# Kernel tuning notes

Hardware: AMD Instinct MI355X
Metric: run time of the kernel (lower is better)

## Reference

```python
import jax, jax.numpy as jnp
import numpy as np

B, F, H, OUT, S = 32768, 256, 128, 64, 6
RELAX, EPS, BN_EPS = 1.5, 1e-05, 1e-05
SQRT_HALF = 0.7071067811865476


def _bn(h, g, b):
    # training-mode BatchNorm1d: biased batch statistics over dim 0
    m = h.mean(axis=0)
    v = h.var(axis=0)
    return (h - m) * jax.lax.rsqrt(v + BN_EPS) * g + b


def _tfrm(x, W, g, b, glu_act=True):
    h = _bn(x @ W, g, b)
    if glu_act:
        d = h.shape[1] // 2
        h = h[:, :d] * jax.nn.sigmoid(h[:, d:])
    return h


def setup_inputs() -> dict:
    key = jax.random.key(0)
    ks = jax.random.split(key, 6)
    f32 = jnp.float32
    return {
        "x": jax.random.normal(ks[0], (B, F), f32),
        "enc_g": jnp.ones((F,), f32), "enc_b": jnp.zeros((F,), f32),
        "W1": jax.random.normal(ks[1], (F, 2 * H), f32) * 0.05,
        "g1": jnp.ones((2 * H,), f32), "b1": jnp.zeros((2 * H,), f32),
        "W2": jax.random.normal(ks[2], (H, 2 * H), f32) * 0.05,
        "g2": jnp.ones((2 * H,), f32), "b2": jnp.zeros((2 * H,), f32),
        "W3": jax.random.normal(ks[3], (S, H, 2 * H), f32) * 0.05,
        "g3": jnp.ones((S, 2 * H), f32), "b3": jnp.zeros((S, 2 * H), f32),
        "W4": jax.random.normal(ks[4], (S, H, 2 * H), f32) * 0.05,
        "g4": jnp.ones((S, 2 * H), f32), "b4": jnp.zeros((S, 2 * H), f32),
        "Wc": jax.random.normal(ks[5], (S - 1, OUT, F), f32) * 0.05,
        "gc": jnp.ones((S - 1, F), f32), "bc": jnp.zeros((S - 1, F), f32),
    }


def reference(x, enc_g, enc_b, W1, g1, b1, W2, g2, b2, W3, g3, b3,
              W4, g4, b4, Wc, gc, bc):
    x = _bn(x, enc_g, enc_b)                      # [B, F]
    masked = x
    compl = jnp.ones((x.shape[0], F), x.dtype)    # complementary aggregated mask
    agg_out, agg_entropy = [], []
    for ni in range(S):
        h = _tfrm(masked, W1, g1, b1)                             # [B, H]
        h = (_tfrm(h, W2, g2, b2) + h) * SQRT_HALF
        h = (_tfrm(h, W3[ni], g3[ni], b3[ni]) + h) * SQRT_HALF
        h = (_tfrm(h, W4[ni], g4[ni], b4[ni]) + h) * SQRT_HALF
        if ni > 0:
            # NOTE: source uses x (not h) here -- replicated faithfully
            agg_out.append(jax.nn.relu(x[:, :OUT]))
        fc = h[:, OUT:]                                           # [B, OUT]
        if ni < S - 1:
            coef = _tfrm(fc, Wc[ni], gc[ni], bc[ni], glu_act=False)  # [B, F]
            mask_values = jax.nn.softmax(coef * compl, axis=1)
            compl = compl * (RELAX - mask_values)
            agg_entropy.append(
                jnp.mean(jnp.sum(-mask_values * jnp.log(mask_values + EPS), axis=1))
                / (S - 1))
            masked = mask_values * x
    out = jnp.sum(jnp.stack(agg_out, axis=0), axis=0)   # [B, OUT]
    entropy = jnp.sum(jnp.stack(agg_entropy))           # scalar
    return (out, entropy)
```

## Files before the change

### kernel.cpp

```cpp
#include <hip/hip_runtime.h>
#include <math.h>

#define BSZ   32768
#define FDIM  256
#define HDIM  128
#define OUTD  64
#define SQRT_HALF 0.70710678118654752f
#define BN_EPS 1e-5f
#define SM_EPS 1e-5f
#define INV_B (1.0f / 32768.0f)
#define NCPY  8
#define SLOT  (NCPY * 512)
#define GRID  1024

#define SWZ(r, cb) ((((r) << 9) + (cb)) ^ (((r) & 7) << 4))

typedef __attribute__((ext_vector_type(8))) short bf16x8;
typedef __attribute__((ext_vector_type(4))) short bf16x4;
typedef __attribute__((ext_vector_type(4))) float f32x4;

__device__ __forceinline__ float b2f(unsigned short u) {
    return __uint_as_float(((unsigned int)u) << 16);
}
__device__ __forceinline__ unsigned short f2b(float f) {
    unsigned int u = __float_as_uint(f);
    u += 0x7fff + ((u >> 16) & 1);
    return (unsigned short)(u >> 16);
}

__device__ __forceinline__ void async16(const void* g, void* l) {
    __builtin_amdgcn_global_load_lds(
        (const __attribute__((address_space(1))) void*)(uintptr_t)g,
        (__attribute__((address_space(3))) void*)(unsigned int)(uintptr_t)l,
        16, 0, 0);
}

__device__ __forceinline__ float cload(const float* p) {
    return __hip_atomic_load(p, __ATOMIC_RELAXED, __HIP_MEMORY_SCOPE_AGENT);
}
__device__ __forceinline__ void catomic_add(float* p, float v) {
    float old = __hip_atomic_fetch_add(p, v, __ATOMIC_RELAXED, __HIP_MEMORY_SCOPE_AGENT);
    asm volatile("" :: "v"(old));
}

__device__ inline float waveMaxAll(float v) {
#pragma unroll
    for (int m = 32; m > 0; m >>= 1) v = fmaxf(v, __shfl_xor(v, m, 64));
    return v;
}
__device__ inline float waveSumAll(float v) {
#pragma unroll
    for (int m = 32; m > 0; m >>= 1) v += __shfl_xor(v, m, 64);
    return v;
}

__device__ __forceinline__ void grid_sync_nf(unsigned int* arr, unsigned int* rel,
                                             unsigned int gen, int bid, int tid) {
    __syncthreads();
    if (tid == 0)
        __hip_atomic_fetch_add(&arr[(bid & 63) << 5], 1u,
                               __ATOMIC_RELAXED, __HIP_MEMORY_SCOPE_AGENT);
    if (bid == 0) {
        if (tid < 64) {
            unsigned int* p = &arr[tid << 5];
            long spin = 0;
            while (__hip_atomic_load(p, __ATOMIC_RELAXED, __HIP_MEMORY_SCOPE_AGENT) < gen * 16u) {
                if (++spin > (1L << 24)) break;
                __builtin_amdgcn_s_sleep(1);
            }
        }
        asm volatile("" ::: "memory");
        __syncthreads();
        if (tid == 0)
            __hip_atomic_store(rel, gen, __ATOMIC_RELAXED, __HIP_MEMORY_SCOPE_AGENT);
    } else {
        if (tid == 0) {
            long spin = 0;
            while (__hip_atomic_load(rel, __ATOMIC_RELAXED, __HIP_MEMORY_SCOPE_AGENT) < gen) {
                if (++spin > (1L << 24)) break;
                __builtin_amdgcn_s_sleep(2);
            }
        }
        asm volatile("" ::: "memory");
    }
    __syncthreads();
}

__device__ __forceinline__ void stage_B(short* Bs, const unsigned short* __restrict__ Wt,
                                        int K, int k0, int wave, int lane) {
    const int sr = lane >> 2;
    const int sc = (lane & 3) * 8;
#pragma unroll
    for (int t = 0; t < 4; ++t) {
        const int wr = wave * 64 + t * 16 + sr;
        async16(Wt + (size_t)wr * K + k0 + sc, (void*)(Bs + (wave * 4 + t) * 512 + lane * 8));
    }
}

__device__ __forceinline__ void gemm_core(const short* buf, short* Bs,
                                          const unsigned short* __restrict__ Wt, int K,
                                          int wave, int lane, f32x4 (&acc)[2][4]) {
    const int fm = lane & 15;
    const int fq = (lane >> 4) * 8;
#pragma unroll
    for (int i = 0; i < 2; ++i)
#pragma unroll
        for (int j = 0; j < 4; ++j)
            acc[i][j] = (f32x4){0.f, 0.f, 0.f, 0.f};

    __syncthreads();

    for (int k0 = 0; k0 < K; k0 += 32) {
        asm volatile("s_waitcnt vmcnt(0)" ::: "memory");
        bf16x8 af[2], bfr[4];
#pragma unroll
        for (int i = 0; i < 2; ++i)
            af[i] = *(const bf16x8*)((const char*)buf + SWZ(i * 16 + fm, (k0 + fq) * 2));
#pragma unroll
        for (int j = 0; j < 4; ++j)
            bfr[j] = *(const bf16x8*)(Bs + (wave * 64 + j * 16 + fm) * 32 + fq);
#pragma unroll
        for (int i = 0; i < 2; ++i)
#pragma unroll
            for (int j = 0; j < 4; ++j)
                acc[i][j] = __builtin_amdgcn_mfma_f32_16x16x32_bf16(af[i], bfr[j], acc[i][j], 0, 0, 0);
        if (k0 + 32 < K) {
            asm volatile("s_waitcnt lgkmcnt(0)" ::: "memory");
            __builtin_amdgcn_sched_barrier(0);
            stage_B(Bs, Wt, K, k0 + 32, wave, lane);
        }
    }
    __syncthreads();
}

__device__ __forceinline__ void stage_epilogue(f32x4 (&acc)[2][4], short* buf,
                                               float* redS, float* redQ,
                                               float* __restrict__ statsOut,
                                               int wave, int lane, int tid, int bcp) {
    const int fm = lane & 15;
    const int row4 = (lane >> 4) * 4;
    const int ocol = wave * 64 + fm;
#pragma unroll
    for (int i = 0; i < 2; ++i)
#pragma unroll
        for (int j = 0; j < 4; ++j)
#pragma unroll
            for (int r = 0; r < 4; ++r)
                *(short*)((char*)buf + SWZ(row4 + i * 16 + r, (ocol + j * 16) * 2)) =
                    (short)f2b(acc[i][j][r]);

#pragma unroll
    for (int j = 0; j < 4; ++j) {
        float s = 0.f, q = 0.f;
#pragma unroll
        for (int i = 0; i < 2; ++i)
#pragma unroll
            for (int r = 0; r < 4; ++r) {
                float v = acc[i][j][r];
                s += v; q += v * v;
            }
        s += __shfl_xor(s, 16, 64); s += __shfl_xor(s, 32, 64);
        q += __shfl_xor(q, 16, 64); q += __shfl_xor(q, 32, 64);
        if (lane < 16) {
            redS[wave * 64 + j * 16 + lane] = s;
            redQ[wave * 64 + j * 16 + lane] = q;
        }
    }
    __syncthreads();
    catomic_add(&statsOut[bcp + tid], redS[tid]);
    catomic_add(&statsOut[bcp + 256 + tid], redQ[tid]);
}

__device__ __forceinline__ void build_tbl_glu(const float* __restrict__ st,
                                              const float* __restrict__ pg,
                                              const float* __restrict__ pb,
                                              int colOff, int K, int tid, float* tbl) {
    if (tid < K) {
        const int ch = colOff + tid;
        const int cg = ch + 128;
        float sA = 0.f, qA = 0.f, sG = 0.f, qG = 0.f;
#pragma unroll
        for (int cp = 0; cp < NCPY; ++cp) {
            const float* p = st + cp * 512;
            sA += cload(p + ch); qA += cload(p + 256 + ch);
            sG += cload(p + cg); qG += cload(p + 256 + cg);
        }
        float ma = sA * INV_B, va = qA * INV_B - ma * ma;
        float scA = pg[ch] * rsqrtf(va + BN_EPS);
        tbl[tid] = scA; tbl[K + tid] = pb[ch] - ma * scA;
        float mg = sG * INV_B, vg = qG * INV_B - mg * mg;
        float scG = pg[cg] * rsqrtf(vg + BN_EPS);
        tbl[2 * K + tid] = scG; tbl[3 * K + tid] = pb[cg] - mg * scG;
    }
    __syncthreads();
}

__device__ __forceinline__ void build_tbl_mask(const float* __restrict__ st,
                                               const float* __restrict__ gcp,
                                               const float* __restrict__ bcp_,
                                               int tid, float* tbl) {
    float s = 0.f, q = 0.f;
#pragma unroll
    for (int cp = 0; cp < NCPY; ++cp) {
        s += cload(st + cp * 512 + tid);
        q += cload(st + cp * 512 + 256 + tid);
    }
    float mean = s * INV_B, var = q * INV_B - mean * mean;
    float scl = gcp[tid] * rsqrtf(var + BN_EPS);
    tbl[tid] = scl;
    tbl[256 + tid] = bcp_[tid] - mean * scl;
    __syncthreads();
}

template <int K, bool RES, bool WH, int RB>
__device__ __forceinline__ void glu_prologue(short* buf, const float* tbl,
                                             int tid, int colOff, bf16x4* h) {
    const int ar = tid >> 3;
    const int ac = (tid & 7) * 4;
#pragma unroll
    for (int c = 0; c < K / 32; ++c) {
        const int kk = c * 32 + ac;
        bf16x4 lo = *(const bf16x4*)((const char*)buf + SWZ(ar, (colOff + kk) * 2));
        bf16x4 hi = *(const bf16x4*)((const char*)buf + SWZ(ar, (colOff + kk + 128) * 2));
        float4 a0 = *(const float4*)&tbl[kk];
        float4 h0 = *(const float4*)&tbl[K + kk];
        float4 g0 = *(const float4*)&tbl[2 * K + kk];
        float4 s0 = *(const float4*)&tbl[3 * K + kk];
        const float scA[4] = {a0.x, a0.y, a0.z, a0.w};
        const float shA[4] = {h0.x, h0.y, h0.z, h0.w};
        const float scG[4] = {g0.x, g0.y, g0.z, g0.w};
        const float shG[4] = {s0.x, s0.y, s0.z, s0.w};
        bf16x4 o4;
#pragma unroll
        for (int e = 0; e < 4; ++e) {
            float na = b2f((unsigned short)lo[e]) * scA[e] + shA[e];
            float ng = b2f((unsigned short)hi[e]) * scG[e] + shG[e];
            float v = na * (1.0f / (1.0f + __expf(-ng)));
            if (RES) v = (v + b2f((unsigned short)h[RB + c][e])) * SQRT_HALF;
            o4[e] = (short)f2b(v);
        }
        *(bf16x4*)((char*)buf + SWZ(ar, kk * 2)) = o4;
        if (WH) h[c] = o4;
    }
}

template <int MODE>
__device__ __forceinline__ void mask_phase(short* buf, const float* tbl,
                                           const unsigned short* __restrict__ xb,
                                           unsigned short* cmpl, float* ent, float* went,
                                           int tid, int wave, int lane, int row0, int bid) {
    const int r = tid >> 3;
    const int cq = tid & 7;
    const size_t grow = (size_t)(row0 + r) * 256;

    float l[32];
    float mx = -1e30f;
#pragma unroll
    for (int e = 0; e < 4; ++e) {
        const int c = cq * 32 + e * 8;
        bf16x8 pv = *(const bf16x8*)((const char*)buf + SWZ(r, c * 2));
        bf16x8 cv;
        if (MODE != 0) cv = *(const bf16x8*)(cmpl + grow + c);
        float4 s0 = *(const float4*)&tbl[c], s1 = *(const float4*)&tbl[c + 4];
        float4 h0 = *(const float4*)&tbl[256 + c], h1 = *(const float4*)&tbl[256 + c + 4];
        const float* sp0 = (const float*)&s0; const float* sp1 = (const float*)&s1;
        const float* hp0 = (const float*)&h0; const float* hp1 = (const float*)&h1;
#pragma unroll
        for (int t = 0; t < 8; ++t) {
            float scl = (t < 4) ? sp0[t] : sp1[t - 4];
            float shf = (t < 4) ? hp0[t] : hp1[t - 4];
            float cl = (MODE != 0) ? b2f((unsigned short)cv[t]) : 1.0f;
            float v = (b2f((unsigned short)pv[t]) * scl + shf) * cl;
            l[e * 8 + t] = v;
            mx = fmaxf(mx, v);
        }
    }
    mx = fmaxf(mx, __shfl_xor(mx, 1, 64));
    mx = fmaxf(mx, __shfl_xor(mx, 2, 64));
    mx = fmaxf(mx, __shfl_xor(mx, 4, 64));

    float ssum = 0.f;
#pragma unroll
    for (int i = 0; i < 32; ++i) { l[i] = __expf(l[i] - mx); ssum += l[i]; }
    ssum += __shfl_xor(ssum, 1, 64);
    ssum += __shfl_xor(ssum, 2, 64);
    ssum += __shfl_xor(ssum, 4, 64);
    const float inv = 1.0f / ssum;

    float et = 0.f;
#pragma unroll
    for (int e = 0; e < 4; ++e) {
        const int c = cq * 32 + e * 8;
        bf16x8 xv, cv2;
        if (MODE != 2) xv = *(const bf16x8*)(xb + grow + c);
        if (MODE == 1) cv2 = *(const bf16x8*)(cmpl + grow + c);
        bf16x8 mo, co;
#pragma unroll
        for (int t = 0; t < 8; ++t) {
            float m = l[e * 8 + t] * inv;
            et -= m * __logf(m + SM_EPS);
            if (MODE != 2) {
                float cl = (MODE == 1) ? b2f((unsigned short)cv2[t]) : 1.0f;
                co[t] = (short)f2b(cl * (1.5f - m));
                mo[t] = (short)f2b(m * b2f((unsigned short)xv[t]));
            }
        }
        if (MODE != 2) {
            *(bf16x8*)(cmpl + grow + c) = co;
            *(bf16x8*)((char*)buf + SWZ(r, c * 2)) = mo;
        }
    }
    et += __shfl_xor(et, 1, 64);
    et += __shfl_xor(et, 2, 64);
    et += __shfl_xor(et, 4, 64);
    float wet = waveSumAll(et) * 0.125f;
    if (lane == 0) went[wave] = wet;
    __syncthreads();
    if (tid == 0) {
        float v = went[0] + went[1] + went[2] + went[3];
        catomic_add(&ent[(bid & 255) << 5], v * (INV_B * 0.2f));
    }
}

__global__ __launch_bounds__(256, 4) void mega(
    const float* __restrict__ x,
    const float* __restrict__ enc_g, const float* __restrict__ enc_b,
    const float* __restrict__ g1, const float* __restrict__ b1,
    const float* __restrict__ g2, const float* __restrict__ b2,
    const float* __restrict__ g3, const float* __restrict__ b3,
    const float* __restrict__ g4, const float* __restrict__ b4,
    const float* __restrict__ gc, const float* __restrict__ bc,
    const float* __restrict__ W1f, const float* __restrict__ W2f,
    const float* __restrict__ W3f, const float* __restrict__ W4f,
    const float* __restrict__ Wcf,
    unsigned short* __restrict__ W1t, unsigned short* __restrict__ W2t,
    unsigned short* __restrict__ W3t, unsigned short* __restrict__ W4t,
    unsigned short* __restrict__ Wct,
    unsigned short* __restrict__ xb, unsigned short* __restrict__ cmpl,
    float* __restrict__ stats, float* __restrict__ ent,
    unsigned int* __restrict__ bar,
    float* __restrict__ out)
{
    __shared__ short buf[32 * 256];
    __shared__ short Bs[256 * 32];
    __shared__ float redS[256], redQ[256];
    __shared__ float tbl[512];
    __shared__ float went[4];

    const int tid  = threadIdx.x;
    const int wave = tid >> 6;
    const int lane = tid & 63;
    const int bid  = blockIdx.x;
    const int row0 = bid * 32;
    const int bcp  = (bid & (NCPY - 1)) * 512;

    unsigned int* rel = bar + 64 * 32;
    unsigned int bgen = 0;
#define GSYNC() do { ++bgen; grid_sync_nf(bar, rel, bgen, bid, tid); } while (0)

    if (bid < 136) {
        const int m = bid >> 3, kz = bid & 7, n = tid;
        const float* src; unsigned short* dst; int K;
        if (m == 0)      { src = W1f;                        dst = W1t;               K = 256; }
        else if (m == 1) { src = W2f;                        dst = W2t;               K = 128; }
        else if (m < 7)  { int i = m - 2;  src = W3f + (size_t)i * 128 * 256; dst = W3t + (size_t)i * 32768; K = 128; }
        else if (m < 12) { int i = m - 7;  src = W4f + (size_t)i * 128 * 256; dst = W4t + (size_t)i * 32768; K = 128; }
        else             { int i = m - 12; src = Wcf + (size_t)i * 64 * 256;  dst = Wct + (size_t)i * 16384; K = 64; }
        const int k0 = kz * 32;
        if (k0 < K)
            for (int k = k0; k < k0 + 32; ++k)
                dst[(size_t)n * K + k] = f2b(src[(size_t)k * 256 + n]);
        __threadfence();
    }
    {
        float* red = (float*)buf;
        const int sub = wave;
        const int c4  = lane << 2;
        float s[4] = {0.f, 0.f, 0.f, 0.f}, q[4] = {0.f, 0.f, 0.f, 0.f};
#pragma unroll 8
        for (int i = 0; i < 8; ++i) {
            const int row = row0 + i * 4 + sub;
            float4 v = *(const float4*)(x + (size_t)row * 256 + c4);
            s[0] += v.x; q[0] += v.x * v.x;
            s[1] += v.y; q[1] += v.y * v.y;
            s[2] += v.z; q[2] += v.z * v.z;
            s[3] += v.w; q[3] += v.w * v.w;
        }
#pragma unroll
        for (int e = 0; e < 4; ++e) {
            red[sub * 512 + c4 + e] = s[e];
            red[sub * 512 + 256 + c4 + e] = q[e];
        }
        __syncthreads();
        float sS = red[tid] + red[512 + tid] + red[1024 + tid] + red[1536 + tid];
        float sQ = red[256 + tid] + red[768 + tid] + red[1280 + tid] + red[1792 + tid];
        catomic_add(&stats[bcp + tid], sS);
        catomic_add(&stats[bcp + 256 + tid], sQ);
    }
    GSYNC();

    stage_B(Bs, W1t, 256, 0, wave, lane);
    {
        float s = 0.f, q = 0.f;
#pragma unroll
        for (int cp = 0; cp < NCPY; ++cp) {
            s += cload(stats + cp * 512 + tid);
            q += cload(stats + cp * 512 + 256 + tid);
        }
        float mean = s * INV_B, var = q * INV_B - mean * mean;
        float scl = enc_g[tid] * rsqrtf(var + BN_EPS);
        tbl[tid] = scl;
        tbl[256 + tid] = enc_b[tid] - mean * scl;
    }
    __syncthreads();
    {
        const int r = tid >> 3, cq = tid & 7;
        const size_t grow = (size_t)(row0 + r) * 256;
#pragma unroll
        for (int e = 0; e < 4; ++e) {
            const int c = cq * 32 + e * 8;
            float4 xa = *(const float4*)(x + grow + c);
            float4 xc = *(const float4*)(x + grow + c + 4);
            const float xv[8] = {xa.x, xa.y, xa.z, xa.w, xc.x, xc.y, xc.z, xc.w};
            float4 s0 = *(const float4*)&tbl[c], s1 = *(const float4*)&tbl[c + 4];
            float4 f0 = *(const float4*)&tbl[256 + c], f1 = *(const float4*)&tbl[256 + c + 4];
            const float sc[8] = {s0.x, s0.y, s0.z, s0.w, s1.x, s1.y, s1.z, s1.w};
            const float sh[8] = {f0.x, f0.y, f0.z, f0.w, f1.x, f1.y, f1.z, f1.w};
            float n[8];
            bf16x8 o8;
#pragma unroll
            for (int t = 0; t < 8; ++t) {
                n[t] = xv[t] * sc[t] + sh[t];
                o8[t] = (short)f2b(n[t]);
            }
            *(bf16x8*)((char*)buf + SWZ(r, c * 2)) = o8;
            *(bf16x8*)(xb + grow + c) = o8;
            if (c < OUTD) {
                float4 o1 = make_float4(5.f * fmaxf(n[0], 0.f), 5.f * fmaxf(n[1], 0.f),
                                        5.f * fmaxf(n[2], 0.f), 5.f * fmaxf(n[3], 0.f));
                float4 o2 = make_float4(5.f * fmaxf(n[4], 0.f), 5.f * fmaxf(n[5], 0.f),
                                        5.f * fmaxf(n[6], 0.f), 5.f * fmaxf(n[7], 0.f));
                *(float4*)(out + (size_t)(row0 + r) * OUTD + c) = o1;
                *(float4*)(out + (size_t)(row0 + r) * OUTD + c + 4) = o2;
            }
        }
    }

    f32x4 acc[2][4];
    bf16x4 h[4];

    for (int ni = 0; ni < 5; ++ni) {
        float* s1 = stats + (size_t)(1 + ni * 5 + 0) * SLOT;
        float* s2 = stats + (size_t)(1 + ni * 5 + 1) * SLOT;
        float* s3 = stats + (size_t)(1 + ni * 5 + 2) * SLOT;
        float* s4 = stats + (size_t)(1 + ni * 5 + 3) * SLOT;
        float* s5 = stats + (size_t)(1 + ni * 5 + 4) * SLOT;

        if (ni > 0) {
            float* s5p = stats + (size_t)(1 + (ni - 1) * 5 + 4) * SLOT;
            build_tbl_mask(s5p, gc + (ni - 1) * 256, bc + (ni - 1) * 256, tid, tbl);
            if (ni == 1)
                mask_phase<0>(buf, tbl, xb, cmpl, ent, went, tid, wave, lane, row0, bid);
            else
                mask_phase<1>(buf, tbl, xb, cmpl, ent, went, tid, wave, lane, row0, bid);
        }
        gemm_core(buf, Bs, W1t, 256, wave, lane, acc);
        stage_epilogue(acc, buf, redS, redQ, s1, wave, lane, tid, bcp);
        stage_B(Bs, W2t, 128, 0, wave, lane);
        GSYNC();

        build_tbl_glu(s1, g1, b1, 0, 128, tid, tbl);
        glu_prologue<128, false, true, 0>(buf, tbl, tid, 0, h);
        gemm_core(buf, Bs, W2t, 128, wave, lane, acc);
        stage_epilogue(acc, buf, redS, redQ, s2, wave, lane, tid, bcp);
        stage_B(Bs, W3t + (size_t)ni * 32768, 128, 0, wave, lane);
        GSYNC();

        build_tbl_glu(s2, g2, b2, 0, 128, tid, tbl);
        glu_prologue<128, true, true, 0>(buf, tbl, tid, 0, h);
        gemm_core(buf, Bs, W3t + (size_t)ni * 32768, 128, wave, lane, acc);
        stage_epilogue(acc, buf, redS, redQ, s3, wave, lane, tid, bcp);
        stage_B(Bs, W4t + (size_t)ni * 32768, 128, 0, wave, lane);
        GSYNC();

        build_tbl_glu(s3, g3 + ni * 256, b3 + ni * 256, 0, 128, tid, tbl);
        glu_prologue<128, true, true, 0>(buf, tbl, tid, 0, h);
        gemm_core(buf, Bs, W4t + (size_t)ni * 32768, 128, wave, lane, acc);
        stage_epilogue(acc, buf, redS, redQ, s4, wave, lane, tid, bcp);
        stage_B(Bs, Wct + (size_t)ni * 16384, 64, 0, wave, lane);
        GSYNC();

        build_tbl_glu(s4, g4 + ni * 256, b4 + ni * 256, 64, 64, tid, tbl);
        glu_prologue<64, true, false, 2>(buf, tbl, tid, 64, h);
        gemm_core(buf, Bs, Wct + (size_t)ni * 16384, 64, wave, lane, acc);
        stage_epilogue(acc, buf, redS, redQ, s5, wave, lane, tid, bcp);
        if (ni < 4) stage_B(Bs, W1t, 256, 0, wave, lane);
        GSYNC();
    }

    build_tbl_mask(stats + (size_t)(1 + 4 * 5 + 4) * SLOT,
                   gc + 4 * 256, bc + 4 * 256, tid, tbl);
    mask_phase<2>(buf, tbl, xb, cmpl, ent, went, tid, wave, lane, row0, bid);
    GSYNC();

    if (bid == 0 && wave == 0) {
        float v = 0.f;
#pragma unroll
        for (int i = 0; i < 4; ++i) v += cload(ent + ((lane + 64 * i) << 5));
        v = waveSumAll(v);
        if (lane == 0) out[(size_t)BSZ * OUTD] = v;
    }
#undef GSYNC
}

__global__ __launch_bounds__(256) void prep_w(
    const float* __restrict__ W1, const float* __restrict__ W2,
    const float* __restrict__ W3, const float* __restrict__ W4,
    const float* __restrict__ Wc,
    unsigned short* __restrict__ W1t, unsigned short* __restrict__ W2t,
    unsigned short* __restrict__ W3t, unsigned short* __restrict__ W4t,
    unsigned short* __restrict__ Wct)
{
    const int m = blockIdx.x, kz = blockIdx.y, n = threadIdx.x;
    const float* src; unsigned short* dst; int K;
    if (m == 0)      { src = W1;                        dst = W1t;               K = 256; }
    else if (m == 1) { src = W2;                        dst = W2t;               K = 128; }
    else if (m < 7)  { int i = m - 2;  src = W3 + (size_t)i * 128 * 256; dst = W3t + (size_t)i * 32768; K = 128; }
    else if (m < 12) { int i = m - 7;  src = W4 + (size_t)i * 128 * 256; dst = W4t + (size_t)i * 32768; K = 128; }
    else             { int i = m - 12; src = Wc + (size_t)i * 64 * 256;  dst = Wct + (size_t)i * 16384; K = 64; }
    const int k0 = kz * 32;
    if (k0 >= K) return;
    for (int k = k0; k < k0 + 32; ++k)
        dst[(size_t)n * K + k] = f2b(src[(size_t)k * 256 + n]);
}

__global__ __launch_bounds__(256) void colstats(const float* __restrict__ X,
                                                float* __restrict__ st0) {
    __shared__ float red[4][512];
    const int sub = threadIdx.x >> 6;
    const int c4  = (threadIdx.x & 63) << 2;
    float s[4] = {0.f, 0.f, 0.f, 0.f}, q[4] = {0.f, 0.f, 0.f, 0.f};
#pragma unroll 8
    for (int i = 0; i < 8; ++i) {
        const int row = blockIdx.x * 32 + i * 4 + sub;
        float4 v = *(const float4*)(X + (size_t)row * 256 + c4);
        s[0] += v.x; q[0] += v.x * v.x;
        s[1] += v.y; q[1] += v.y * v.y;
        s[2] += v.z; q[2] += v.z * v.z;
        s[3] += v.w; q[3] += v.w * v.w;
    }
#pragma unroll
    for (int e = 0; e < 4; ++e) {
        red[sub][c4 + e] = s[e];
        red[sub][256 + c4 + e] = q[e];
    }
    __syncthreads();
    const int t = threadIdx.x;
    const int cp = (blockIdx.x & (NCPY - 1)) * 512;
    float sS = red[0][t] + red[1][t] + red[2][t] + red[3][t];
    float sQ = red[0][256 + t] + red[1][256 + t] + red[2][256 + t] + red[3][256 + t];
    atomicAdd(&st0[cp + t], sS);
    atomicAdd(&st0[cp + 256 + t], sQ);
}

__global__ __launch_bounds__(256) void norm_x(const float* __restrict__ x,
                                              const float* __restrict__ st0,
                                              const float* __restrict__ g,
                                              const float* __restrict__ b,
                                              unsigned short* __restrict__ xb,
                                              float* __restrict__ out) {
    const int i4 = blockIdx.x * 256 + threadIdx.x;
    const int row = i4 >> 6, c4 = (i4 & 63) << 2;
    float4 xv = *(const float4*)(x + (size_t)row * 256 + c4);
    float sS[4] = {0.f, 0.f, 0.f, 0.f}, sQ[4] = {0.f, 0.f, 0.f, 0.f};
#pragma unroll
    for (int cp = 0; cp < NCPY; ++cp) {
        float4 a = *(const float4*)&st0[cp * 512 + c4];
        float4 q = *(const float4*)&st0[cp * 512 + 256 + c4];
        sS[0] += a.x; sS[1] += a.y; sS[2] += a.z; sS[3] += a.w;
        sQ[0] += q.x; sQ[1] += q.y; sQ[2] += q.z; sQ[3] += q.w;
    }
    float4 gv = *(const float4*)&g[c4];
    float4 bv = *(const float4*)&b[c4];
    const float* xp = (const float*)&xv;
    const float* gp = (const float*)&gv; const float* bp = (const float*)&bv;
    float n[4];
    ushort4 ob;
    unsigned short* obp = (unsigned short*)&ob;
#pragma unroll
    for (int e = 0; e < 4; ++e) {
        float mean = sS[e] * INV_B;
        float var  = sQ[e] * INV_B - mean * mean;
        float sc   = gp[e] * rsqrtf(var + BN_EPS);
        float sh   = bp[e] - mean * sc;
        n[e] = xp[e] * sc + sh;
        obp[e] = f2b(n[e]);
    }
    *(ushort4*)(xb + (size_t)row * 256 + c4) = ob;
    if (c4 < OUTD) {
        float4 ov = make_float4(5.0f * fmaxf(n[0], 0.f), 5.0f * fmaxf(n[1], 0.f),
                                5.0f * fmaxf(n[2], 0.f), 5.0f * fmaxf(n[3], 0.f));
        *(float4*)(out + (size_t)row * OUTD + c4) = ov;
    }
}

__device__ __forceinline__ void gemm_epilogue(
    f32x4 (&acc)[2][4], int row0, int wave, int lane, int tid, int bcp,
    float* redS, float* redQ,
    unsigned short* __restrict__ Pout, float* __restrict__ statsOut)
{
    const int fm = lane & 15;
    const int orow = row0 + (lane >> 4) * 4;
    const int ocol = wave * 64 + fm;
#pragma unroll
    for (int i = 0; i < 2; ++i)
#pragma unroll
        for (int j = 0; j < 4; ++j)
#pragma unroll
            for (int r = 0; r < 4; ++r)
                Pout[(size_t)(orow + i * 16 + r) * 256 + (ocol + j * 16)] = f2b(acc[i][j][r]);

#pragma unroll
    for (int j = 0; j < 4; ++j) {
        float s = 0.f, q = 0.f;
#pragma unroll
        for (int i = 0; i < 2; ++i)
#pragma unroll
            for (int r = 0; r < 4; ++r) {
                float v = acc[i][j][r];
                s += v; q += v * v;
            }
        s += __shfl_xor(s, 16, 64); s += __shfl_xor(s, 32, 64);
        q += __shfl_xor(q, 16, 64); q += __shfl_xor(q, 32, 64);
        if (lane < 16) {
            redS[wave * 64 + j * 16 + lane] = s;
            redQ[wave * 64 + j * 16 + lane] = q;
        }
    }
    __syncthreads();
    atomicAdd(&statsOut[bcp + tid], redS[tid]);
    atomicAdd(&statsOut[bcp + 256 + tid], redQ[tid]);
}

__global__ __launch_bounds__(256) void gemm_bf16(
    const unsigned short* __restrict__ A,
    const unsigned short* __restrict__ Wt, int K,
    unsigned short* __restrict__ P,
    float* __restrict__ statsOut)
{
    __shared__ short As[32 * 32];
    __shared__ short Bs[256 * 32];
    __shared__ float redS[256], redQ[256];

    const int tid  = threadIdx.x;
    const int wave = tid >> 6;
    const int lane = tid & 63;
    const int row0 = blockIdx.x * 32;
    const int bcp  = (blockIdx.x & (NCPY - 1)) * 512;

    const int sr = lane >> 2;
    const int sc = (lane & 3) * 8;
    const int fm = lane & 15;
    const int fq = (lane >> 4) * 8;

    f32x4 acc[2][4];
// ... 271 lines not shown
            float4 h0 = *(const float4*)&tShA[kk];
            float4 g0 = *(const float4*)&tScG[kk];
            float4 s0 = *(const float4*)&tShG[kk];
            float scA[4] = {a0.x, a0.y, a0.z, a0.w};
            float shA[4] = {h0.x, h0.y, h0.z, h0.w};
            float scG[4] = {g0.x, g0.y, g0.z, g0.w};
            float shG[4] = {s0.x, s0.y, s0.z, s0.w};

            bf16x4 o4;
#pragma unroll
            for (int e = 0; e < 4; ++e) {
                float na = b2f((unsigned short)lo[e]) * scA[e] + shA[e];
                float ng = b2f((unsigned short)hi[e]) * scG[e] + shG[e];
                float v = na * (1.0f / (1.0f + __expf(-ng)));
                if (RES) v = (v + b2f((unsigned short)rv[e])) * SQRT_HALF;
                o4[e] = (short)f2b(v);
            }
            *(bf16x4*)(As + ar * 32 + ac) = o4;
            if (WRITE_H)
                *(bf16x4*)(hOut + grow * 128 + kk) = o4;
        }
        __syncthreads();

        bf16x8 af[2], bfr[4];
#pragma unroll
        for (int i = 0; i < 2; ++i)
            af[i] = *(const bf16x8*)(As + (i * 16 + fm) * 32 + fq);
#pragma unroll
        for (int j = 0; j < 4; ++j)
            bfr[j] = *(const bf16x8*)(Bs + (wave * 64 + j * 16 + fm) * 32 + fq);
#pragma unroll
        for (int i = 0; i < 2; ++i)
#pragma unroll
            for (int j = 0; j < 4; ++j)
                acc[i][j] = __builtin_amdgcn_mfma_f32_16x16x32_bf16(af[i], bfr[j], acc[i][j], 0, 0, 0);
        __syncthreads();
    }

    gemm_epilogue(acc, row0, wave, lane, tid, bcp, redS, redQ, Pout, statsOut);
}

__global__ __launch_bounds__(256) void coef_ent(const unsigned short* __restrict__ Pc,
                                                const float* __restrict__ stats,
                                                const float* __restrict__ gc,
                                                const float* __restrict__ bc,
                                                const unsigned short* __restrict__ cmpl,
                                                float* __restrict__ ent) {
    const int w    = threadIdx.x >> 6;
    const int lane = threadIdx.x & 63;
    const int row  = blockIdx.x * 4 + w;
    const int c    = lane << 2;
    __shared__ float went[4];

    float sS[4] = {0.f, 0.f, 0.f, 0.f}, sQ[4] = {0.f, 0.f, 0.f, 0.f};
#pragma unroll
    for (int cp = 0; cp < NCPY; ++cp) {
        float4 a = *(const float4*)&stats[cp * 512 + c];
        float4 q = *(const float4*)&stats[cp * 512 + 256 + c];
        sS[0] += a.x; sS[1] += a.y; sS[2] += a.z; sS[3] += a.w;
        sQ[0] += q.x; sQ[1] += q.y; sQ[2] += q.z; sQ[3] += q.w;
    }
    float4 gv = *(const float4*)&gc[c];
    float4 bv = *(const float4*)&bc[c];
    const float* gvv = (const float*)&gv; const float* bvv = (const float*)&bv;

    float scl[4], shf[4];
#pragma unroll
    for (int e = 0; e < 4; ++e) {
        float mean = sS[e] * INV_B, var = sQ[e] * INV_B - mean * mean;
        scl[e] = gvv[e] * rsqrtf(var + BN_EPS);
        shf[e] = bvv[e] - mean * scl[e];
    }

    const size_t idx = (size_t)row * 256 + c;
    ushort4 pu = *(const ushort4*)(Pc + idx);
    const unsigned short* puv = (const unsigned short*)&pu;
    ushort4 cu = *(const ushort4*)(cmpl + idx);
    const unsigned short* cuv = (const unsigned short*)&cu;

    float l[4];
#pragma unroll
    for (int e = 0; e < 4; ++e)
        l[e] = (b2f(puv[e]) * scl[e] + shf[e]) * b2f(cuv[e]);

    float mx = waveMaxAll(fmaxf(fmaxf(l[0], l[1]), fmaxf(l[2], l[3])));
    float e0 = __expf(l[0] - mx), e1 = __expf(l[1] - mx),
          e2 = __expf(l[2] - mx), e3 = __expf(l[3] - mx);
    float inv = 1.0f / waveSumAll(e0 + e1 + e2 + e3);

    float m[4] = {e0 * inv, e1 * inv, e2 * inv, e3 * inv};

    float et = -m[0] * __logf(m[0] + SM_EPS) - m[1] * __logf(m[1] + SM_EPS)
             - m[2] * __logf(m[2] + SM_EPS) - m[3] * __logf(m[3] + SM_EPS);
    et = waveSumAll(et);
    if (lane == 0) went[w] = et;
    __syncthreads();
    if (threadIdx.x == 0) {
        float v = went[0] + went[1] + went[2] + went[3];
        atomicAdd(&ent[(blockIdx.x & 255) << 5], v * (INV_B * 0.2f));
    }
}

__global__ __launch_bounds__(64) void write_ent(const float* __restrict__ ent,
                                                float* __restrict__ dst) {
    const int lane = threadIdx.x;
    float v = 0.f;
#pragma unroll
    for (int i = 0; i < 4; ++i) v += ent[(lane + 64 * i) << 5];
    v = waveSumAll(v);
    if (lane == 0) dst[0] = v;
}

extern "C" void kernel_launch(void* const* d_in, const int* in_sizes, int n_in,
                              void* d_out, int out_size, void* d_ws, size_t ws_size,
                              hipStream_t stream) {
    const float* x     = (const float*)d_in[0];
    const float* enc_g = (const float*)d_in[1];
    const float* enc_b = (const float*)d_in[2];
    const float* W1 = (const float*)d_in[3];
    const float* g1 = (const float*)d_in[4];
    const float* b1 = (const float*)d_in[5];
    const float* W2 = (const float*)d_in[6];
    const float* g2 = (const float*)d_in[7];
    const float* b2 = (const float*)d_in[8];
    const float* W3 = (const float*)d_in[9];
    const float* g3 = (const float*)d_in[10];
    const float* b3 = (const float*)d_in[11];
    const float* W4 = (const float*)d_in[12];
    const float* g4 = (const float*)d_in[13];
    const float* b4 = (const float*)d_in[14];
    const float* Wc = (const float*)d_in[15];
    const float* gc = (const float*)d_in[16];
    const float* bc = (const float*)d_in[17];
    float* out = (float*)d_out;

    const size_t NBF = (size_t)BSZ * FDIM;
    const size_t NBH = (size_t)BSZ * HDIM;

    unsigned short* xb     = (unsigned short*)d_ws;
    unsigned short* masked = xb + NBF;
    unsigned short* Pb1    = masked + NBF;
    unsigned short* h1     = Pb1 + NBF;
    unsigned short* h2     = h1 + NBH;
    unsigned short* h3     = h2 + NBH;
    unsigned short* cmpl   = h3 + NBH;
    unsigned short* W1t    = cmpl + NBF;
    unsigned short* W2t    = W1t + 65536;
    unsigned short* W3t    = W2t + 32768;
    unsigned short* W4t    = W3t + 163840;
    unsigned short* Wct    = W4t + 163840;
    float* stats = (float*)(Wct + 81920);
    float* ent   = stats + 26 * SLOT;
    unsigned int* bar = (unsigned int*)masked;

    unsigned short* Pb2 = masked;

    static int s_ok = -1;
    if (s_ok < 0) {
        int occ = 0, mpc = 0, dev = 0;
        hipGetDevice(&dev);
        hipDeviceProp_t prop;
        if (hipGetDeviceProperties(&prop, dev) == hipSuccess) mpc = prop.multiProcessorCount;
        if (hipOccupancyMaxActiveBlocksPerMultiprocessor(
                &occ, reinterpret_cast<const void*>(mega), 256, 0) != hipSuccess) occ = 0;
        s_ok = (occ >= 4 && occ * mpc >= GRID) ? 1 : 0;
    }

    hipMemsetAsync(stats, 0, (26 * SLOT + 256 * 32) * sizeof(float), stream);

    if (s_ok) {
        hipMemsetAsync(bar, 0, 65 * 32 * sizeof(unsigned int), stream);
        mega<<<GRID, 256, 0, stream>>>(
            x, enc_g, enc_b, g1, b1, g2, b2, g3, b3, g4, b4, gc, bc,
            W1, W2, W3, W4, Wc, W1t, W2t, W3t, W4t, Wct,
            xb, cmpl, stats, ent, bar, out);
        return;
    }

    prep_w<<<dim3(17, 8), 256, 0, stream>>>(W1, W2, W3, W4, Wc, W1t, W2t, W3t, W4t, Wct);
    colstats<<<1024, 256, 0, stream>>>(x, stats);
    norm_x<<<8192, 256, 0, stream>>>(x, stats, enc_g, enc_b, xb, out);

    for (int ni = 0; ni < 5; ++ni) {
        float* s1 = stats + (size_t)(1 + ni * 5 + 0) * SLOT;
        float* s2 = stats + (size_t)(1 + ni * 5 + 1) * SLOT;
        float* s3 = stats + (size_t)(1 + ni * 5 + 2) * SLOT;
        float* s4 = stats + (size_t)(1 + ni * 5 + 3) * SLOT;
        float* s5 = stats + (size_t)(1 + ni * 5 + 4) * SLOT;

        if (ni == 0) {
            gemm_bf16<<<1024, 256, 0, stream>>>(xb, W1t, 256, Pb1, s1);
        } else {
            float* s5p = stats + (size_t)(1 + (ni - 1) * 5 + 4) * SLOT;
            if (ni == 1)
                gemm_mask<0><<<1024, 256, 0, stream>>>(
                    Pb1, s5p, gc, bc, xb, cmpl, ent, W1t, Pb1, s1);
            else
                gemm_mask<1><<<1024, 256, 0, stream>>>(
                    Pb1, s5p, gc + (ni - 1) * 256, bc + (ni - 1) * 256,
                    xb, cmpl, ent, W1t, Pb1, s1);
        }

        gemm_glu<false, true><<<1024, 256, 0, stream>>>(
            Pb1, s1, g1, b1, nullptr, 0, W2t, 128, Pb2, s2, h1);
        gemm_glu<true, true><<<1024, 256, 0, stream>>>(
            Pb2, s2, g2, b2, h1, 0, W3t + (size_t)ni * 32768, 128, Pb1, s3, h2);
        gemm_glu<true, true><<<1024, 256, 0, stream>>>(
            Pb1, s3, g3 + ni * 256, b3 + ni * 256, h2, 0,
            W4t + (size_t)ni * 32768, 128, Pb2, s4, h3);
        gemm_glu<true, false><<<1024, 256, 0, stream>>>(
            Pb2, s4, g4 + ni * 256, b4 + ni * 256, h3 + 64, 64,
            Wct + (size_t)ni * 16384, 64, Pb1, s5, nullptr);
    }

    coef_ent<<<BSZ / 4, 256, 0, stream>>>(
        Pb1, stats + (size_t)(1 + 4 * 5 + 4) * SLOT,
        gc + 4 * 256, bc + 4 * 256, cmpl, ent);

    write_ent<<<1, 64, 0, stream>>>(ent, out + (size_t)BSZ * OUTD);
}
```

Before: 563.7 us.

## Double block size to 64 rows and 8 waves sharing each staged weight tile

```diff
diff --git a/kernel.cpp b/kernel.cpp
--- a/kernel.cpp
+++ b/kernel.cpp
@@ -11,7 +11,7 @@
 #define INV_B (1.0f / 32768.0f)
 #define NCPY  8
 #define SLOT  (NCPY * 512)
-#define GRID  1024
+#define GRID  512
 
 #define SWZ(r, cb) ((((r) << 9) + (cb)) ^ (((r) & 7) << 4))
 
@@ -64,7 +64,7 @@
         if (tid < 64) {
             unsigned int* p = &arr[tid << 5];
             long spin = 0;
-            while (__hip_atomic_load(p, __ATOMIC_RELAXED, __HIP_MEMORY_SCOPE_AGENT) < gen * 16u) {
+            while (__hip_atomic_load(p, __ATOMIC_RELAXED, __HIP_MEMORY_SCOPE_AGENT) < gen * 8u) {
                 if (++spin > (1L << 24)) break;
                 __builtin_amdgcn_s_sleep(1);
             }
@@ -91,9 +91,9 @@
     const int sr = lane >> 2;
     const int sc = (lane & 3) * 8;
 #pragma unroll
-    for (int t = 0; t < 4; ++t) {
-        const int wr = wave * 64 + t * 16 + sr;
-        async16(Wt + (size_t)wr * K + k0 + sc, (void*)(Bs + (wave * 4 + t) * 512 + lane * 8));
+    for (int t = 0; t < 2; ++t) {
+        const int wr = wave * 32 + t * 16 + sr;
+        async16(Wt + (size_t)wr * K + k0 + sc, (void*)(Bs + (wave * 2 + t) * 512 + lane * 8));
     }
 }
 
@@ -102,35 +102,31 @@
                                           int wave, int lane, f32x4 (&acc)[2][4]) {
     const int fm = lane & 15;
     const int fq = (lane >> 4) * 8;
+    const int cw = wave & 3;
+    const int rh = wave >> 2;
 #pragma unroll
     for (int i = 0; i < 2; ++i)
 #pragma unroll
         for (int j = 0; j < 4; ++j)
             acc[i][j] = (f32x4){0.f, 0.f, 0.f, 0.f};
 
-    __syncthreads();
-
     for (int k0 = 0; k0 < K; k0 += 32) {
-        asm volatile("s_waitcnt vmcnt(0)" ::: "memory");
+        __syncthreads();
         bf16x8 af[2], bfr[4];
 #pragma unroll
         for (int i = 0; i < 2; ++i)
-            af[i] = *(const bf16x8*)((const char*)buf + SWZ(i * 16 + fm, (k0 + fq) * 2));
+            af[i] = *(const bf16x8*)((const char*)buf + SWZ(rh * 32 + i * 16 + fm, (k0 + fq) * 2));
 #pragma unroll
         for (int j = 0; j < 4; ++j)
-            bfr[j] = *(const bf16x8*)(Bs + (wave * 64 + j * 16 + fm) * 32 + fq);
+            bfr[j] = *(const bf16x8*)(Bs + (cw * 64 + j * 16 + fm) * 32 + fq);
 #pragma unroll
         for (int i = 0; i < 2; ++i)
 #pragma unroll
             for (int j = 0; j < 4; ++j)
                 acc[i][j] = __builtin_amdgcn_mfma_f32_16x16x32_bf16(af[i], bfr[j], acc[i][j], 0, 0, 0);
-        if (k0 + 32 < K) {
-            asm volatile("s_waitcnt lgkmcnt(0)" ::: "memory");
-            __builtin_amdgcn_sched_barrier(0);
-            stage_B(Bs, Wt, K, k0 + 32, wave, lane);
-        }
-    }
-    __syncthreads();
+        __syncthreads();
+        if (k0 + 32 < K) stage_B(Bs, Wt, K, k0 + 32, wave, lane);
+    }
 }
 
 __device__ __forceinline__ void stage_epilogue(f32x4 (&acc)[2][4], short* buf,
@@ -138,8 +134,10 @@
                                                float* __restrict__ statsOut,
                                                int wave, int lane, int tid, int bcp) {
     const int fm = lane & 15;
-    const int row4 = (lane >> 4) * 4;
-    const int ocol = wave * 64 + fm;
+    const int cw = wave & 3;
+    const int rh = wave >> 2;
+    const int row4 = rh * 32 + (lane >> 4) * 4;
+    const int ocol = cw * 64 + fm;
 #pragma unroll
     for (int i = 0; i < 2; ++i)
 #pragma unroll
@@ -162,13 +160,15 @@
         s += __shfl_xor(s, 16, 64); s += __shfl_xor(s, 32, 64);
         q += __shfl_xor(q, 16, 64); q += __shfl_xor(q, 32, 64);
         if (lane < 16) {
-            redS[wave * 64 + j * 16 + lane] = s;
-            redQ[wave * 64 + j * 16 + lane] = q;
-        }
-    }
-    __syncthreads();
-    catomic_add(&statsOut[bcp + tid], redS[tid]);
-    catomic_add(&statsOut[bcp + 256 + tid], redQ[tid]);
+            redS[rh * 256 + cw * 64 + j * 16 + lane] = s;
+            redQ[rh * 256 + cw * 64 + j * 16 + lane] = q;
+        }
+    }
+    __syncthreads();
+    float v;
+    if (tid < 256) v = redS[tid] + redS[tid + 256];
+    else           { int c = tid - 256; v = redQ[c] + redQ[c + 256]; }
+    catomic_add(&statsOut[bcp + tid], v);
 }
 
 __device__ __forceinline__ void build_tbl_glu(const float* __restrict__ st,
@@ -199,16 +199,18 @@
                                                const float* __restrict__ gcp,
                                                const float* __restrict__ bcp_,
                                                int tid, float* tbl) {
-    float s = 0.f, q = 0.f;
-#pragma unroll
-    for (int cp = 0; cp < NCPY; ++cp) {
-        s += cload(st + cp * 512 + tid);
-        q += cload(st + cp * 512 + 256 + tid);
-    }
-    float mean = s * INV_B, var = q * INV_B - mean * mean;
-    float scl = gcp[tid] * rsqrtf(var + BN_EPS);
-    tbl[tid] = scl;
-    tbl[256 + tid] = bcp_[tid] - mean * scl;
+    if (tid < 256) {
+        float s = 0.f, q = 0.f;
+#pragma unroll
+        for (int cp = 0; cp < NCPY; ++cp) {
+            s += cload(st + cp * 512 + tid);
+            q += cload(st + cp * 512 + 256 + tid);
+        }
+        float mean = s * INV_B, var = q * INV_B - mean * mean;
+        float scl = gcp[tid] * rsqrtf(var + BN_EPS);
+        tbl[tid] = scl;
+        tbl[256 + tid] = bcp_[tid] - mean * scl;
+    }
     __syncthreads();
 }
 
@@ -317,12 +319,14 @@
     if (lane == 0) went[wave] = wet;
     __syncthreads();
     if (tid == 0) {
-        float v = went[0] + went[1] + went[2] + went[3];
+        float v = 0.f;
+#pragma unroll
+        for (int w8 = 0; w8 < 8; ++w8) v += went[w8];
         catomic_add(&ent[(bid & 255) << 5], v * (INV_B * 0.2f));
     }
 }
 
-__global__ __launch_bounds__(256, 4) void mega(
+__global__ __launch_bounds__(512, 2) void mega(
     const float* __restrict__ x,
     const float* __restrict__ enc_g, const float* __restrict__ enc_b,
     const float* __restrict__ g1, const float* __restrict__ b1,
@@ -341,17 +345,17 @@
     unsigned int* __restrict__ bar,
     float* __restrict__ out)
 {
-    __shared__ short buf[32 * 256];
+    __shared__ short buf[64 * 256];
     __shared__ short Bs[256 * 32];
-    __shared__ float redS[256], redQ[256];
+    __shared__ float redS[512], redQ[512];
     __shared__ float tbl[512];
-    __shared__ float went[4];
+    __shared__ float went[8];
 
     const int tid  = threadIdx.x;
     const int wave = tid >> 6;
     const int lane = tid & 63;
     const int bid  = blockIdx.x;
-    const int row0 = bid * 32;
+    const int row0 = bid * 64;
     const int bcp  = (bid & (NCPY - 1)) * 512;
 
     unsigned int* rel = bar + 64 * 32;
@@ -359,17 +363,19 @@
 #define GSYNC() do { ++bgen; grid_sync_nf(bar, rel, bgen, bid, tid); } while (0)
 
     if (bid < 136) {
-        const int m = bid >> 3, kz = bid & 7, n = tid;
-        const float* src; unsigned short* dst; int K;
-        if (m == 0)      { src = W1f;                        dst = W1t;               K = 256; }
-        else if (m == 1) { src = W2f;                        dst = W2t;               K = 128; }
-        else if (m < 7)  { int i = m - 2;  src = W3f + (size_t)i * 128 * 256; dst = W3t + (size_t)i * 32768; K = 128; }
-        else if (m < 12) { int i = m - 7;  src = W4f + (size_t)i * 128 * 256; dst = W4t + (size_t)i * 32768; K = 128; }
-        else             { int i = m - 12; src = Wcf + (size_t)i * 64 * 256;  dst = Wct + (size_t)i * 16384; K = 64; }
-        const int k0 = kz * 32;
-        if (k0 < K)
-            for (int k = k0; k < k0 + 32; ++k)
-                dst[(size_t)n * K + k] = f2b(src[(size_t)k * 256 + n]);
+        if (tid < 256) {
+            const int m = bid >> 3, kz = bid & 7, n = tid;
+            const float* src; unsigned short* dst; int K;
+            if (m == 0)      { src = W1f;                        dst = W1t;               K = 256; }
+            else if (m == 1) { src = W2f;                        dst = W2t;               K = 128; }
+            else if (m < 7)  { int i = m - 2;  src = W3f + (size_t)i * 128 * 256; dst = W3t + (size_t)i * 32768; K = 128; }
+            else if (m < 12) { int i = m - 7;  src = W4f + (size_t)i * 128 * 256; dst = W4t + (size_t)i * 32768; K = 128; }
+            else             { int i = m - 12; src = Wcf + (size_t)i * 64 * 256;  dst = Wct + (size_t)i * 16384; K = 64; }
+            const int k0 = kz * 32;
+            if (k0 < K)
+                for (int k = k0; k < k0 + 32; ++k)
+                    dst[(size_t)n * K + k] = f2b(src[(size_t)k * 256 + n]);
+        }
         __threadfence();
     }
     {
@@ -379,7 +385,7 @@
         float s[4] = {0.f, 0.f, 0.f, 0.f}, q[4] = {0.f, 0.f, 0.f, 0.f};
 #pragma unroll 8
         for (int i = 0; i < 8; ++i) {
-            const int row = row0 + i * 4 + sub;
+            const int row = row0 + i * 8 + sub;
             float4 v = *(const float4*)(x + (size_t)row * 256 + c4);
             s[0] += v.x; q[0] += v.x * v.x;
             s[1] += v.y; q[1] += v.y * v.y;
@@ -392,15 +398,15 @@
             red[sub * 512 + 256 + c4 + e] = q[e];
         }
         __syncthreads();
-        float sS = red[tid] + red[512 + tid] + red[1024 + tid] + red[1536 + tid];
-        float sQ = red[256 + tid] + red[768 + tid] + red[1280 + tid] + red[1792 + tid];
-        catomic_add(&stats[bcp + tid], sS);
-        catomic_add(&stats[bcp + 256 + tid], sQ);
+        float v = 0.f;
+#pragma unroll
+        for (int s8 = 0; s8 < 8; ++s8) v += red[s8 * 512 + tid];
+        catomic_add(&stats[bcp + tid], v);
     }
     GSYNC();
 
     stage_B(Bs, W1t, 256, 0, wave, lane);
-    {
+    if (tid < 256) {
         float s = 0.f, q = 0.f;
 #pragma unroll
         for (int cp = 0; cp < NCPY; ++cp) {
@@ -1098,15 +1104,15 @@
         hipDeviceProp_t prop;
         if (hipGetDeviceProperties(&prop, dev) == hipSuccess) mpc = prop.multiProcessorCount;
         if (hipOccupancyMaxActiveBlocksPerMultiprocessor(
-                &occ, reinterpret_cast<const void*>(mega), 256, 0) != hipSuccess) occ = 0;
-        s_ok = (occ >= 4 && occ * mpc >= GRID) ? 1 : 0;
+                &occ, reinterpret_cast<const void*>(mega), 512, 0) != hipSuccess) occ = 0;
+        s_ok = (occ >= 2 && occ * mpc >= GRID) ? 1 : 0;
     }
 
     hipMemsetAsync(stats, 0, (26 * SLOT + 256 * 32) * sizeof(float), stream);
 
     if (s_ok) {
         hipMemsetAsync(bar, 0, 65 * 32 * sizeof(unsigned int), stream);
-        mega<<<GRID, 256, 0, stream>>>(
+        mega<<<GRID, 512, 0, stream>>>(
             x, enc_g, enc_b, g1, b1, g2, b2, g3, b3, g4, b4, gc, bc,
             W1, W2, W3, W4, Wc, W1t, W2t, W3t, W4t, Wct,
             xb, cmpl, stats, ent, bar, out);
```

Result: no change. 572.8 us (+1.6%).

## Replace atomic BN stat accumulation with per-block partials and two-phase grid reduction

Applied to the files above, without the earlier changes.

```diff
diff --git a/kernel.cpp b/kernel.cpp
--- a/kernel.cpp
+++ b/kernel.cpp
@@ -12,6 +12,7 @@
 #define NCPY  8
 #define SLOT  (NCPY * 512)
 #define GRID  1024
+#define PARTN (1024 * 512)
 
 #define SWZ(r, cb) ((((r) << 9) + (cb)) ^ (((r) & 7) << 4))
 
@@ -54,12 +55,14 @@
     return v;
 }
 
-__device__ __forceinline__ void grid_sync_nf(unsigned int* arr, unsigned int* rel,
-                                             unsigned int gen, int bid, int tid) {
-    __syncthreads();
-    if (tid == 0)
+__device__ __forceinline__ void grid_sync_f(unsigned int* arr, unsigned int* rel,
+                                            unsigned int gen, int bid, int tid) {
+    __syncthreads();
+    if (tid == 0) {
+        __threadfence();
         __hip_atomic_fetch_add(&arr[(bid & 63) << 5], 1u,
                                __ATOMIC_RELAXED, __HIP_MEMORY_SCOPE_AGENT);
+    }
     if (bid == 0) {
         if (tid < 64) {
             unsigned int* p = &arr[tid << 5];
@@ -86,6 +89,24 @@
     __syncthreads();
 }
 
+__device__ __forceinline__ void reduce_partials(const float* part, float* slot,
+                                                int bid, int tid) {
+    if (bid < 8) {
+        __threadfence();
+        float s0 = 0.f, s1 = 0.f;
+        const float* base = part + (size_t)bid * 128 * 512 + 2 * tid;
+#pragma unroll 8
+        for (int i = 0; i < 128; ++i) {
+            float2 v = *(const float2*)(base + (size_t)i * 512);
+            s0 += v.x; s1 += v.y;
+        }
+        float2 o = make_float2(s0, s1);
+        unsigned long long u = *(unsigned long long*)&o;
+        __hip_atomic_store((unsigned long long*)(slot + (size_t)bid * 512 + 2 * tid), u,
+                           __ATOMIC_RELAXED, __HIP_MEMORY_SCOPE_AGENT);
+    }
+}
+
 __device__ __forceinline__ void stage_B(short* Bs, const unsigned short* __restrict__ Wt,
                                         int K, int k0, int wave, int lane) {
     const int sr = lane >> 2;
@@ -135,8 +156,8 @@
 
 __device__ __forceinline__ void stage_epilogue(f32x4 (&acc)[2][4], short* buf,
                                                float* redS, float* redQ,
-                                               float* __restrict__ statsOut,
-                                               int wave, int lane, int tid, int bcp) {
+                                               float* __restrict__ partRow,
+                                               int wave, int lane, int tid) {
     const int fm = lane & 15;
     const int row4 = (lane >> 4) * 4;
     const int ocol = wave * 64 + fm;
@@ -167,8 +188,11 @@
         }
     }
     __syncthreads();
-    catomic_add(&statsOut[bcp + tid], redS[tid]);
-    catomic_add(&statsOut[bcp + 256 + tid], redQ[tid]);
+    float2 o;
+    int off;
+    if (tid < 128) { o = make_float2(redS[2 * tid], redS[2 * tid + 1]); off = 2 * tid; }
+    else { int t = tid - 128; o = make_float2(redQ[2 * t], redQ[2 * t + 1]); off = 256 + 2 * t; }
+    *(float2*)(partRow + off) = o;
 }
 
 __device__ __forceinline__ void build_tbl_glu(const float* __restrict__ st,
@@ -339,6 +363,7 @@
     unsigned short* __restrict__ xb, unsigned short* __restrict__ cmpl,
     float* __restrict__ stats, float* __restrict__ ent,
     unsigned int* __restrict__ bar,
+    float* __restrict__ partials,
     float* __restrict__ out)
 {
     __shared__ short buf[32 * 256];
@@ -352,11 +377,14 @@
     const int lane = tid & 63;
     const int bid  = blockIdx.x;
     const int row0 = bid * 32;
-    const int bcp  = (bid & (NCPY - 1)) * 512;
 
     unsigned int* rel = bar + 64 * 32;
     unsigned int bgen = 0;
-#define GSYNC() do { ++bgen; grid_sync_nf(bar, rel, bgen, bid, tid); } while (0)
+    int pp = 0;
+    float* pb0 = partials;
+    float* pb1 = partials + PARTN;
+#define GSYNC() do { ++bgen; grid_sync_f(bar, rel, bgen, bid, tid); } while (0)
+#define PBUF (pp ? pb1 : pb0)
 
     if (bid < 136) {
         const int m = bid >> 3, kz = bid & 7, n = tid;
@@ -370,7 +398,6 @@
         if (k0 < K)
             for (int k = k0; k < k0 + 32; ++k)
                 dst[(size_t)n * K + k] = f2b(src[(size_t)k * 256 + n]);
-        __threadfence();
     }
     {
         float* red = (float*)buf;
@@ -394,10 +421,17 @@
         __syncthreads();
         float sS = red[tid] + red[512 + tid] + red[1024 + tid] + red[1536 + tid];
         float sQ = red[256 + tid] + red[768 + tid] + red[1280 + tid] + red[1792 + tid];
-        catomic_add(&stats[bcp + tid], sS);
-        catomic_add(&stats[bcp + 256 + tid], sQ);
+        red[tid] = sS; red[256 + tid] = sQ;
+        __syncthreads();
+        float2 o; int off;
+        if (tid < 128) { o = make_float2(red[2 * tid], red[2 * tid + 1]); off = 2 * tid; }
+        else { int t = tid - 128; o = make_float2(red[256 + 2 * t], red[256 + 2 * t + 1]); off = 256 + 2 * t; }
+        *(float2*)(PBUF + (size_t)bid * 512 + off) = o;
     }
     GSYNC();
+    reduce_partials(PBUF, stats, bid, tid);
+    GSYNC();
+    pp ^= 1;
 
     stage_B(Bs, W1t, 256, 0, wave, lane);
     {
@@ -448,6 +482,7 @@
 
     f32x4 acc[2][4];
     bf16x4 h[4];
+    float* partRowBase = nullptr;
 
     for (int ni = 0; ni < 5; ++ni) {
         float* s1 = stats + (size_t)(1 + ni * 5 + 0) * SLOT;
@@ -465,37 +500,57 @@
                 mask_phase<1>(buf, tbl, xb, cmpl, ent, went, tid, wave, lane, row0, bid);
         }
         gemm_core(buf, Bs, W1t, 256, wave, lane, acc);
-        stage_epilogue(acc, buf, redS, redQ, s1, wave, lane, tid, bcp);
+        partRowBase = PBUF + (size_t)bid * 512;
+        stage_epilogue(acc, buf, redS, redQ, partRowBase, wave, lane, tid);
         stage_B(Bs, W2t, 128, 0, wave, lane);
         GSYNC();
+        reduce_partials(PBUF, s1, bid, tid);
+        GSYNC();
+        pp ^= 1;
 
         build_tbl_glu(s1, g1, b1, 0, 128, tid, tbl);
         glu_prologue<128, false, true, 0>(buf, tbl, tid, 0, h);
         gemm_core(buf, Bs, W2t, 128, wave, lane, acc);
-        stage_epilogue(acc, buf, redS, redQ, s2, wave, lane, tid, bcp);
+        partRowBase = PBUF + (size_t)bid * 512;
+        stage_epilogue(acc, buf, redS, redQ, partRowBase, wave, lane, tid);
         stage_B(Bs, W3t + (size_t)ni * 32768, 128, 0, wave, lane);
         GSYNC();
+        reduce_partials(PBUF, s2, bid, tid);
+        GSYNC();
+        pp ^= 1;
 
         build_tbl_glu(s2, g2, b2, 0, 128, tid, tbl);
         glu_prologue<128, true, true, 0>(buf, tbl, tid, 0, h);
         gemm_core(buf, Bs, W3t + (size_t)ni * 32768, 128, wave, lane, acc);
-        stage_epilogue(acc, buf, redS, redQ, s3, wave, lane, tid, bcp);
+        partRowBase = PBUF + (size_t)bid * 512;
+        stage_epilogue(acc, buf, redS, redQ, partRowBase, wave, lane, tid);
         stage_B(Bs, W4t + (size_t)ni * 32768, 128, 0, wave, lane);
         GSYNC();
+        reduce_partials(PBUF, s3, bid, tid);
+        GSYNC();
+        pp ^= 1;
 
         build_tbl_glu(s3, g3 + ni * 256, b3 + ni * 256, 0, 128, tid, tbl);
         glu_prologue<128, true, true, 0>(buf, tbl, tid, 0, h);
         gemm_core(buf, Bs, W4t + (size_t)ni * 32768, 128, wave, lane, acc);
-        stage_epilogue(acc, buf, redS, redQ, s4, wave, lane, tid, bcp);
+        partRowBase = PBUF + (size_t)bid * 512;
+        stage_epilogue(acc, buf, redS, redQ, partRowBase, wave, lane, tid);
         stage_B(Bs, Wct + (size_t)ni * 16384, 64, 0, wave, lane);
         GSYNC();
+        reduce_partials(PBUF, s4, bid, tid);
+        GSYNC();
+        pp ^= 1;
 
         build_tbl_glu(s4, g4 + ni * 256, b4 + ni * 256, 64, 64, tid, tbl);
         glu_prologue<64, true, false, 2>(buf, tbl, tid, 64, h);
         gemm_core(buf, Bs, Wct + (size_t)ni * 16384, 64, wave, lane, acc);
-        stage_epilogue(acc, buf, redS, redQ, s5, wave, lane, tid, bcp);
+        partRowBase = PBUF + (size_t)bid * 512;
+        stage_epilogue(acc, buf, redS, redQ, partRowBase, wave, lane, tid);
         if (ni < 4) stage_B(Bs, W1t, 256, 0, wave, lane);
         GSYNC();
+        reduce_partials(PBUF, s5, bid, tid);
+        GSYNC();
+        pp ^= 1;
     }
 
     build_tbl_mask(stats + (size_t)(1 + 4 * 5 + 4) * SLOT,
@@ -511,6 +566,7 @@
         if (lane == 0) out[(size_t)BSZ * OUTD] = v;
     }
 #undef GSYNC
+#undef PBUF
 }
 
 __global__ __launch_bounds__(256) void prep_w(
@@ -1088,15 +1144,17 @@
     float* stats = (float*)(Wct + 81920);
     float* ent   = stats + 26 * SLOT;
     unsigned int* bar = (unsigned int*)masked;
+    float* partials = (float*)Pb1;
 
     unsigned short* Pb2 = masked;
 
     static int s_ok = -1;
     if (s_ok < 0) {
-        int occ = 0, mpc = 0, dev = 0;
+        int occ = 0, mpc = 256, dev = 0;
         hipGetDevice(&dev);
         hipDeviceProp_t prop;
-        if (hipGetDeviceProperties(&prop, dev) == hipSuccess) mpc = prop.multiProcessorCount;
+        if (hipGetDeviceProperties(&prop, dev) == hipSuccess && prop.multiProcessorCount > 0)
+            mpc = prop.multiProcessorCount;
         if (hipOccupancyMaxActiveBlocksPerMultiprocessor(
                 &occ, reinterpret_cast<const void*>(mega), 256, 0) != hipSuccess) occ = 0;
         s_ok = (occ >= 4 && occ * mpc >= GRID) ? 1 : 0;
@@ -1109,7 +1167,7 @@
         mega<<<GRID, 256, 0, stream>>>(
             x, enc_g, enc_b, g1, b1, g2, b2, g3, b3, g4, b4, gc, bc,
             W1, W2, W3, W4, Wc, W1t, W2t, W3t, W4t, Wct,
-            xb, cmpl, stats, ent, bar, out);
+            xb, cmpl, stats, ent, bar, partials, out);
         return;
     }
 
```

After: 560.5 us. Within noise of the previous version (-0.6%).
